# Performance work log

Measured on AMD Instinct MI355X. Metric: run time of the kernel, lower is better.

## Reference

```python
import jax, jax.numpy as jnp
import numpy as np

# irreps '128x0e + 64x1o + 32x2e' as (mul, l) pairs; ir.dim = 2*l+1
IRREPS = [(128, 0), (64, 1), (32, 2)]
B, NE = 256, 400
E_DIM, FF_DIM, HID, OUT = 32, 64, 256, 1
D = sum(m * (2 * l + 1) for m, l in IRREPS)      # 480 = irreps total dim
NCOP = sum(m for m, _ in IRREPS)                 # 224 = n_copies / inv_dim
EPS = 1e-8


def _mlp3(x, W1, b1, W2, b2, W3, b3):
    # MLP(n_layers=3): Linear+SiLU, Linear+SiLU, Linear
    h = jax.nn.silu(x @ W1 + b1)
    h = jax.nn.silu(h @ W2 + b2)
    return h @ W3 + b3


def setup_inputs() -> dict:
    key = jax.random.key(0)
    ks = jax.random.split(key, 16)

    def lin(k, i, o):
        return jax.random.normal(k, (i, o), jnp.float32) / np.float32(np.sqrt(i))

    cond_dim = E_DIM + FF_DIM            # 96
    inv_in = NCOP + FF_DIM               # 288
    return {
        "h_abs_full": jax.random.normal(ks[0], (B, D), jnp.float32),
        "e_feat": jax.random.normal(ks[1], (NE, E_DIM), jnp.float32),
        "field_abs_feat": jax.random.normal(ks[2], (B, FF_DIM), jnp.float32),
        # EnergyIrrepModulation MLP: cond_dim -> HID -> HID -> NCOP
        "mW1": lin(ks[3], cond_dim, HID), "mb1": jnp.zeros((HID,), jnp.float32),
        "mW2": lin(ks[4], HID, HID),      "mb2": jnp.zeros((HID,), jnp.float32),
        "mW3": lin(ks[5], HID, NCOP),     "mb3": jnp.zeros((NCOP,), jnp.float32),
        # out_mlp: inv_dim + ff -> HID -> HID -> OUT
        "oW1": lin(ks[6], inv_in, HID),   "ob1": jnp.zeros((HID,), jnp.float32),
        "oW2": lin(ks[7], HID, HID),      "ob2": jnp.zeros((HID,), jnp.float32),
        "oW3": lin(ks[8], HID, OUT),      "ob3": jnp.zeros((OUT,), jnp.float32),
    }


def reference(h_abs_full, e_feat, field_abs_feat,
              mW1, mb1, mW2, mb2, mW3, mb3,
              oW1, ob1, oW2, ob2, oW3, ob3):
    Bn = h_abs_full.shape[0]
    nE = e_feat.shape[0]
    ff = field_abs_feat.shape[-1]

    # cond: [B, nE, e_dim + ff]
    cond = jnp.concatenate([
        jnp.broadcast_to(e_feat[None], (Bn, nE, e_feat.shape[-1])),
        jnp.broadcast_to(field_abs_feat[:, None], (Bn, nE, ff)),
    ], axis=-1)

    # gates: [B, nE, n_copies]
    gates = _mlp3(cond, mW1, mb1, mW2, mb2, mW3, mb3)

    # Fused per-irrep broadcast gating + invariant (L2-norm) reduction.
    # h_mod[b,e, block] = x[b, block] * gate[b,e, copy]; inv = sqrt(mean(h_mod^2, dim) + eps)
    outs = []
    xoff, goff = 0, 0
    for mul, l in IRREPS:
        dim = 2 * l + 1
        xb = h_abs_full[:, xoff:xoff + mul * dim].reshape(Bn, 1, mul, dim)
        gb = gates[:, :, goff:goff + mul][..., None]          # [B, nE, mul, 1]
        m = xb * gb                                           # [B, nE, mul, dim]
        if l == 0:
            outs.append(m[..., 0])                            # scalars pass through
        else:
            outs.append(jnp.sqrt(jnp.mean(m * m, axis=-1) + EPS))
        xoff += mul * dim
        goff += mul

    inv = jnp.concatenate(
        outs + [jnp.broadcast_to(field_abs_feat[:, None], (Bn, nE, ff))], axis=-1
    )  # [B, nE, n_copies + ff]

    return _mlp3(inv, oW1, ob1, oW2, ob2, oW3, ob3)           # [B, nE, out_dim]
```

## Files before the change

kernel.cpp:

```cpp
#include <hip/hip_runtime.h>
#include <math.h>

#define BB 256
#define NE 400
#define NP (BB * NE)
#define HID 256
#define NCOP 224
#define DIN 480
#define MBLK 64
#define NBLK (NP / MBLK)

typedef _Float16 half8 __attribute__((ext_vector_type(8)));
typedef _Float16 half4 __attribute__((ext_vector_type(4)));
typedef float f4 __attribute__((ext_vector_type(4)));

static __device__ __forceinline__ float silu_f(float x) {
    return x / (1.0f + __expf(-x));
}

static __device__ __forceinline__ int swz(int row, int colbyte) {
    return (row * 512 + colbyte) ^ ((row & 7) << 4);
}

__global__ void precompute_kernel(const float* __restrict__ h_abs,
                                  const float* __restrict__ e_feat,
                                  const float* __restrict__ field,
                                  const float* __restrict__ mW1,
                                  const float* __restrict__ mb1,
                                  const float* __restrict__ oW1,
                                  const float* __restrict__ ob1,
                                  float* __restrict__ E1,
                                  float* __restrict__ F1,
                                  float* __restrict__ Fo,
                                  float* __restrict__ S)
{
    int r = blockIdx.x;
    int t = threadIdx.x;
    if (r < NE) {
        float a = 0.f;
        #pragma unroll
        for (int k = 0; k < 32; ++k) a += e_feat[r * 32 + k] * mW1[k * HID + t];
        E1[r * HID + t] = a;
    } else if (r < NE + BB) {
        int b = r - NE;
        float a = mb1[t];
        #pragma unroll
        for (int k = 0; k < 64; ++k) a += field[b * 64 + k] * mW1[(32 + k) * HID + t];
        F1[b * HID + t] = a;
    } else if (r < NE + 2 * BB) {
        int b = r - NE - BB;
        float a = ob1[t];
        #pragma unroll
        for (int k = 0; k < 64; ++k) a += field[b * 64 + k] * oW1[(224 + k) * HID + t];
        Fo[b * HID + t] = a;
    } else {
        int b = r - NE - 2 * BB;
        if (t < 64) {
            const float* x = h_abs + b * DIN + 128 + t * 3;
            S[b * 96 + t] = (x[0]*x[0] + x[1]*x[1] + x[2]*x[2]) * (1.0f / 3.0f);
        } else if (t < 96) {
            int c = t - 64;
            const float* x = h_abs + b * DIN + 320 + c * 5;
            float s = 0.f;
            #pragma unroll
            for (int d = 0; d < 5; ++d) s += x[d] * x[d];
            S[b * 96 + t] = s * 0.2f;
        }
    }
}

__global__ void pack_weights(const float* __restrict__ mW2, const float* __restrict__ mW3,
                             const float* __restrict__ oW1, const float* __restrict__ oW2,
                             _Float16* __restrict__ PB2, _Float16* __restrict__ PB3,
                             _Float16* __restrict__ PO1, _Float16* __restrict__ PO2)
{
    int blk = blockIdx.x;
    int l = threadIdx.x;
    const float* W; _Float16* P; int LD;
    if (blk < 128)      { W = mW2; P = PB2; LD = 256; }
    else if (blk < 240) { blk -= 128; W = mW3; P = PB3; LD = 224; }
    else if (blk < 352) { blk -= 240; W = oW1; P = PO1; LD = 256; }
    else                { blk -= 352; W = oW2; P = PO2; LD = 256; }
    int KST = (P == PO1) ? 7 : 8;
    int nt = blk / KST, ks = blk - nt * KST;
    int n  = nt * 16 + (l & 15);
    int k0 = ks * 32 + (l >> 4) * 8;
    half8 v;
    #pragma unroll
    for (int j = 0; j < 8; ++j) v[j] = (_Float16)W[(size_t)(k0 + j) * LD + n];
    *(half8*)&P[(size_t)(blk * 64 + l) * 8] = v;
}

template<int KST, bool TWO>
static __device__ __forceinline__ void mma_phase(const half8* __restrict__ Wp,
                                                 const char* actp, int lane,
                                                 int tile0, f4 acc[4][2])
{
    half8 bf0[KST], bf1[TWO ? KST : 1];
    #pragma unroll
    for (int ks = 0; ks < KST; ++ks)
        bf0[ks] = Wp[(tile0 * KST + ks) * 64 + lane];
    if (TWO) {
        #pragma unroll
        for (int ks = 0; ks < KST; ++ks)
            bf1[ks] = Wp[((tile0 + 8) * KST + ks) * 64 + lane];
    }

    #pragma unroll
    for (int mt = 0; mt < 4; ++mt) {
        acc[mt][0] = (f4){0.f, 0.f, 0.f, 0.f};
        acc[mt][1] = (f4){0.f, 0.f, 0.f, 0.f};
    }

    #pragma unroll
    for (int ks = 0; ks < KST; ++ks) {
        int kb = ks * 64 + ((lane >> 4) << 4);
        half8 a[4];
        #pragma unroll
        for (int mt = 0; mt < 4; ++mt) {
            int row = mt * 16 + (lane & 15);
            a[mt] = *(const half8*)(actp + ((row * 512 + kb) ^ ((row & 7) << 4)));
        }
        #pragma unroll
        for (int mt = 0; mt < 4; ++mt)
            acc[mt][0] = __builtin_amdgcn_mfma_f32_16x16x32_f16(bf0[ks], a[mt], acc[mt][0], 0, 0, 0);
        if (TWO) {
            #pragma unroll
            for (int mt = 0; mt < 4; ++mt)
                acc[mt][1] = __builtin_amdgcn_mfma_f32_16x16x32_f16(bf1[ks], a[mt], acc[mt][1], 0, 0, 0);
        }
    }
}

__global__ __launch_bounds__(512, 1)
void fused_mfma(const float* __restrict__ h_abs,
                const float* __restrict__ mb2, const float* __restrict__ mb3,
                const float* __restrict__ ob2,
                const float* __restrict__ oW3, const float* __restrict__ ob3,
                const float* __restrict__ E1, const float* __restrict__ F1,
                const float* __restrict__ Fo, const float* __restrict__ S,
                const half8* __restrict__ PB2, const half8* __restrict__ PB3,
                const half8* __restrict__ PO1, const half8* __restrict__ PO2,
                float* __restrict__ out)
{
    __shared__ char act[MBLK * 512];
    __shared__ float sred[8][64];

    const int t    = threadIdx.x;
    const int lane = t & 63;
    const int w    = t >> 6;
    const int p0   = blockIdx.x * MBLK;
    const int lr   = lane & 15;
    const int lq   = lane >> 4;

    const int b0 = p0 / NE;
    const int r0 = p0 - b0 * NE;

    {
        #pragma unroll
        for (int i = 0; i < 4; ++i) {
            int c   = i * 512 + t;
            int row = c >> 5;
            int c0  = (c & 31) * 8;
            int e = r0 + row;
            int b = b0;
            if (e >= NE) { e -= NE; b += 1; }
            const f4* ep = (const f4*)&E1[e * HID + c0];
            const f4* fp = (const f4*)&F1[b * HID + c0];
            f4 e0 = ep[0], e1 = ep[1];
            f4 f0 = fp[0], f1 = fp[1];
            half8 hv;
            #pragma unroll
            for (int j = 0; j < 4; ++j) hv[j]     = (_Float16)silu_f(e0[j] + f0[j]);
            #pragma unroll
            for (int j = 0; j < 4; ++j) hv[4 + j] = (_Float16)silu_f(e1[j] + f1[j]);
            *(half8*)(act + swz(row, c0 * 2)) = hv;
        }
    }
    __syncthreads();

    f4 acc[4][2];

    mma_phase<8, true>(PB2, act, lane, w, acc);
    __syncthreads();
    #pragma unroll
    for (int ntj = 0; ntj < 2; ++ntj) {
        int n0 = (w + ntj * 8) * 16 + lq * 4;
        f4 bias = *(const f4*)&mb2[n0];
        #pragma unroll
        for (int mt = 0; mt < 4; ++mt) {
            int row = mt * 16 + lr;
            half4 hv;
            #pragma unroll
            for (int r = 0; r < 4; ++r)
                hv[r] = (_Float16)silu_f(acc[mt][ntj][r] + bias[r]);
            *(half4*)(act + swz(row, n0 * 2)) = hv;
        }
    }
    __syncthreads();

    if (w < 6) mma_phase<8, true >(PB3, act, lane, w, acc);
    else       mma_phase<8, false>(PB3, act, lane, w, acc);
    __syncthreads();
    #pragma unroll
    for (int ntj = 0; ntj < 2; ++ntj) {
        int tile = w + ntj * 8;
        if (tile < 14) {
            int n0 = tile * 16 + lq * 4;
            f4 bias = *(const f4*)&mb3[n0];
            #pragma unroll
            for (int mt = 0; mt < 4; ++mt) {
                int row = mt * 16 + lr;
                int b = b0 + ((r0 + row) >= NE);
                half4 hv;
                if (n0 < 128) {
                    f4 xh = *(const f4*)&h_abs[b * DIN + n0];
                    #pragma unroll
                    for (int r = 0; r < 4; ++r)
                        hv[r] = (_Float16)(xh[r] * (acc[mt][ntj][r] + bias[r]));
                } else {
                    f4 sv = *(const f4*)&S[b * 96 + (n0 - 128)];
                    #pragma unroll
                    for (int r = 0; r < 4; ++r) {
                        float g = acc[mt][ntj][r] + bias[r];
                        hv[r] = (_Float16)sqrtf(g * g * sv[r] + 1e-8f);
                    }
                }
                *(half4*)(act + swz(row, n0 * 2)) = hv;
            }
        }
    }
    __syncthreads();

    mma_phase<7, true>(PO1, act, lane, w, acc);
    __syncthreads();
    #pragma unroll
    for (int ntj = 0; ntj < 2; ++ntj) {
        int n0 = (w + ntj * 8) * 16 + lq * 4;
        #pragma unroll
        for (int mt = 0; mt < 4; ++mt) {
            int row = mt * 16 + lr;
            int b = b0 + ((r0 + row) >= NE);
            f4 fo = *(const f4*)&Fo[b * HID + n0];
            half4 hv;
            #pragma unroll
            for (int r = 0; r < 4; ++r)
                hv[r] = (_Float16)silu_f(acc[mt][ntj][r] + fo[r]);
            *(half4*)(act + swz(row, n0 * 2)) = hv;
        }
    }
    __syncthreads();

    mma_phase<8, true>(PO2, act, lane, w, acc);
    {
        float partial[4] = {0.f, 0.f, 0.f, 0.f};
        #pragma unroll
        for (int ntj = 0; ntj < 2; ++ntj) {
            int n0 = (w + ntj * 8) * 16 + lq * 4;
            f4 bias = *(const f4*)&ob2[n0];
            f4 wv   = *(const f4*)&oW3[n0];
            #pragma unroll
            for (int mt = 0; mt < 4; ++mt)
                #pragma unroll
                for (int r = 0; r < 4; ++r)
                    partial[mt] += silu_f(acc[mt][ntj][r] + bias[r]) * wv[r];
        }
        #pragma unroll
        for (int mt = 0; mt < 4; ++mt) {
            float s = partial[mt];
            s += __shfl_xor(s, 16, 64);
            s += __shfl_xor(s, 32, 64);
            if (lq == 0) sred[w][mt * 16 + lr] = s;
        }
    }
    __syncthreads();
    if (t < 64) {
        float s = ob3[0];
        #pragma unroll
        for (int ww = 0; ww < 8; ++ww) s += sred[ww][t];
        out[p0 + t] = s;
    }
}

extern "C" void kernel_launch(void* const* d_in, const int* in_sizes, int n_in,
                              void* d_out, int out_size, void* d_ws, size_t ws_size,
                              hipStream_t stream) {
    const float* h_abs  = (const float*)d_in[0];
    const float* e_feat = (const float*)d_in[1];
    const float* field  = (const float*)d_in[2];
    const float* mW1 = (const float*)d_in[3];
    const float* mb1 = (const float*)d_in[4];
    const float* mW2 = (const float*)d_in[5];
    const float* mb2 = (const float*)d_in[6];
    const float* mW3 = (const float*)d_in[7];
    const float* mb3 = (const float*)d_in[8];
    const float* oW1 = (const float*)d_in[9];
    const float* ob1 = (const float*)d_in[10];
    const float* oW2 = (const float*)d_in[11];
    const float* ob2 = (const float*)d_in[12];
    const float* oW3 = (const float*)d_in[13];
    const float* ob3 = (const float*)d_in[14];
    float* out = (float*)d_out;

    float* ws = (float*)d_ws;
    float* E1 = ws;
    float* F1 = E1 + NE * HID;
    float* Fo = F1 + BB * HID;
    float* S  = Fo + BB * HID;
    _Float16* PB2 = (_Float16*)(S + BB * 96);
    _Float16* PB3 = PB2 + 16 * 8 * 64 * 8;
    _Float16* PO1 = PB3 + 14 * 8 * 64 * 8;
    _Float16* PO2 = PO1 + 16 * 7 * 64 * 8;

    precompute_kernel<<<NE + 3 * BB, 256, 0, stream>>>(
        h_abs, e_feat, field, mW1, mb1, oW1, ob1, E1, F1, Fo, S);

    pack_weights<<<480, 64, 0, stream>>>(
        mW2, mW3, oW1, oW2, PB2, PB3, PO1, PO2);

    fused_mfma<<<NBLK, 512, 0, stream>>>(
        h_abs, mb2, mb3, ob2, oW3, ob3,
        E1, F1, Fo, S,
        (const half8*)PB2, (const half8*)PB3, (const half8*)PO1, (const half8*)PO2,
        out);
}
```

Before: 111.5 us.

## Halve row tile to 32 with 4-wave blocks and fold biases into accumulators

Each block now handles 32 rows instead of 64, using 256 threads (4 waves) instead of 512. Each wave computes 4 output column tiles over 2 row tiles, in two MFMA passes per layer. Bias and Fo values are loaded straight into the accumulators before the MFMAs, which removes the separate zeroing and the bias adds in the epilogues. The aim is more blocks for better load balance and lower LDS use, at the cost of twice as many weight-fragment reads per output row, since each block reuses weights over fewer rows.

```diff
diff --git a/kernel.cpp b/kernel.cpp
--- a/kernel.cpp
+++ b/kernel.cpp
@@ -7,7 +7,7 @@
 #define HID 256
 #define NCOP 224
 #define DIN 480
-#define MBLK 64
+#define MBLK 32
 #define NBLK (NP / MBLK)
 
 typedef _Float16 half8 __attribute__((ext_vector_type(8)));
@@ -92,47 +92,41 @@
 }
 
 template<int KST, bool TWO>
-static __device__ __forceinline__ void mma_phase(const half8* __restrict__ Wp,
-                                                 const char* actp, int lane,
-                                                 int tile0, f4 acc[4][2])
+static __device__ __forceinline__ void mma_pass(const half8* __restrict__ Wp,
+                                                const char* actp, int lane,
+                                                int tileA, f4 acc[2][2])
 {
-    half8 bf0[KST], bf1[TWO ? KST : 1];
+    half8 bfA[KST], bfB[TWO ? KST : 1];
     #pragma unroll
     for (int ks = 0; ks < KST; ++ks)
-        bf0[ks] = Wp[(tile0 * KST + ks) * 64 + lane];
+        bfA[ks] = Wp[(tileA * KST + ks) * 64 + lane];
     if (TWO) {
         #pragma unroll
         for (int ks = 0; ks < KST; ++ks)
-            bf1[ks] = Wp[((tile0 + 8) * KST + ks) * 64 + lane];
-    }
-
-    #pragma unroll
-    for (int mt = 0; mt < 4; ++mt) {
-        acc[mt][0] = (f4){0.f, 0.f, 0.f, 0.f};
-        acc[mt][1] = (f4){0.f, 0.f, 0.f, 0.f};
+            bfB[ks] = Wp[((tileA + 4) * KST + ks) * 64 + lane];
     }
 
     #pragma unroll
     for (int ks = 0; ks < KST; ++ks) {
         int kb = ks * 64 + ((lane >> 4) << 4);
-        half8 a[4];
-        #pragma unroll
-        for (int mt = 0; mt < 4; ++mt) {
+        half8 a[2];
+        #pragma unroll
+        for (int mt = 0; mt < 2; ++mt) {
             int row = mt * 16 + (lane & 15);
             a[mt] = *(const half8*)(actp + ((row * 512 + kb) ^ ((row & 7) << 4)));
         }
         #pragma unroll
-        for (int mt = 0; mt < 4; ++mt)
-            acc[mt][0] = __builtin_amdgcn_mfma_f32_16x16x32_f16(bf0[ks], a[mt], acc[mt][0], 0, 0, 0);
+        for (int mt = 0; mt < 2; ++mt)
+            acc[mt][0] = __builtin_amdgcn_mfma_f32_16x16x32_f16(bfA[ks], a[mt], acc[mt][0], 0, 0, 0);
         if (TWO) {
             #pragma unroll
-            for (int mt = 0; mt < 4; ++mt)
-                acc[mt][1] = __builtin_amdgcn_mfma_f32_16x16x32_f16(bf1[ks], a[mt], acc[mt][1], 0, 0, 0);
-        }
-    }
-}
-
-__global__ __launch_bounds__(512, 1)
+            for (int mt = 0; mt < 2; ++mt)
+                acc[mt][1] = __builtin_amdgcn_mfma_f32_16x16x32_f16(bfB[ks], a[mt], acc[mt][1], 0, 0, 0);
+        }
+    }
+}
+
+__global__ __launch_bounds__(256, 1)
 void fused_mfma(const float* __restrict__ h_abs,
                 const float* __restrict__ mb2, const float* __restrict__ mb3,
                 const float* __restrict__ ob2,
@@ -144,7 +138,7 @@
                 float* __restrict__ out)
 {
     __shared__ char act[MBLK * 512];
-    __shared__ float sred[8][64];
+    __shared__ float sred[4][32];
 
     const int t    = threadIdx.x;
     const int lane = t & 63;
@@ -159,7 +153,7 @@
     {
         #pragma unroll
         for (int i = 0; i < 4; ++i) {
-            int c   = i * 512 + t;
+            int c   = i * 256 + t;
             int row = c >> 5;
             int c0  = (c & 31) * 8;
             int e = r0 + row;
@@ -179,51 +173,71 @@
     }
     __syncthreads();
 
-    f4 acc[4][2];
-
-    mma_phase<8, true>(PB2, act, lane, w, acc);
-    __syncthreads();
-    #pragma unroll
-    for (int ntj = 0; ntj < 2; ++ntj) {
-        int n0 = (w + ntj * 8) * 16 + lq * 4;
-        f4 bias = *(const f4*)&mb2[n0];
-        #pragma unroll
-        for (int mt = 0; mt < 4; ++mt) {
+    f4 accA[2][2], accB[2][2];
+
+    #pragma unroll
+    for (int j = 0; j < 2; ++j) {
+        f4 bA = *(const f4*)&mb2[(w + 4 * j) * 16 + lq * 4];
+        f4 bB = *(const f4*)&mb2[(w + 8 + 4 * j) * 16 + lq * 4];
+        #pragma unroll
+        for (int mt = 0; mt < 2; ++mt) { accA[mt][j] = bA; accB[mt][j] = bB; }
+    }
+    mma_pass<8, true>(PB2, act, lane, w,     accA);
+    mma_pass<8, true>(PB2, act, lane, w + 8, accB);
+    __syncthreads();
+    #pragma unroll
+    for (int g = 0; g < 4; ++g) {
+        int tile = w + 4 * g;
+        const f4 (*acc)[2] = (g < 2) ? accA : accB;
+        int j = g & 1;
+        int n0 = tile * 16 + lq * 4;
+        #pragma unroll
+        for (int mt = 0; mt < 2; ++mt) {
             int row = mt * 16 + lr;
             half4 hv;
             #pragma unroll
             for (int r = 0; r < 4; ++r)
-                hv[r] = (_Float16)silu_f(acc[mt][ntj][r] + bias[r]);
+                hv[r] = (_Float16)silu_f(acc[mt][j][r]);
             *(half4*)(act + swz(row, n0 * 2)) = hv;
         }
     }
     __syncthreads();
 
-    if (w < 6) mma_phase<8, true >(PB3, act, lane, w, acc);
-    else       mma_phase<8, false>(PB3, act, lane, w, acc);
-    __syncthreads();
-    #pragma unroll
-    for (int ntj = 0; ntj < 2; ++ntj) {
-        int tile = w + ntj * 8;
+    #pragma unroll
+    for (int j = 0; j < 2; ++j) {
+        int tA = w + 4 * j, tB = w + 8 + 4 * j;
+        f4 bA = *(const f4*)&mb3[tA * 16 + lq * 4];
+        f4 bB = (tB < 14) ? *(const f4*)&mb3[tB * 16 + lq * 4] : (f4){0,0,0,0};
+        #pragma unroll
+        for (int mt = 0; mt < 2; ++mt) { accA[mt][j] = bA; accB[mt][j] = bB; }
+    }
+    mma_pass<8, true>(PB3, act, lane, w, accA);
+    if (w < 2) mma_pass<8, true >(PB3, act, lane, w + 8, accB);
+    else       mma_pass<8, false>(PB3, act, lane, w + 8, accB);
+    __syncthreads();
+    #pragma unroll
+    for (int g = 0; g < 4; ++g) {
+        int tile = w + 4 * g;
         if (tile < 14) {
+            const f4 (*acc)[2] = (g < 2) ? accA : accB;
+            int j = g & 1;
             int n0 = tile * 16 + lq * 4;
-            f4 bias = *(const f4*)&mb3[n0];
-            #pragma unroll
-            for (int mt = 0; mt < 4; ++mt) {
+            #pragma unroll
+            for (int mt = 0; mt < 2; ++mt) {
                 int row = mt * 16 + lr;
                 int b = b0 + ((r0 + row) >= NE);
                 half4 hv;
-                if (n0 < 128) {
+                if (tile < 8) {
                     f4 xh = *(const f4*)&h_abs[b * DIN + n0];
                     #pragma unroll
                     for (int r = 0; r < 4; ++r)
-                        hv[r] = (_Float16)(xh[r] * (acc[mt][ntj][r] + bias[r]));
+                        hv[r] = (_Float16)(xh[r] * acc[mt][j][r]);
                 } else {
                     f4 sv = *(const f4*)&S[b * 96 + (n0 - 128)];
                     #pragma unroll
                     for (int r = 0; r < 4; ++r) {
-                        float g = acc[mt][ntj][r] + bias[r];
-                        hv[r] = (_Float16)sqrtf(g * g * sv[r] + 1e-8f);
+                        float g2 = acc[mt][j][r];
+                        hv[r] = (_Float16)sqrtf(g2 * g2 * sv[r] + 1e-8f);
                     }
                 }
                 *(half4*)(act + swz(row, n0 * 2)) = hv;
@@ -232,41 +246,65 @@
     }
     __syncthreads();
 
-    mma_phase<7, true>(PO1, act, lane, w, acc);
-    __syncthreads();
-    #pragma unroll
-    for (int ntj = 0; ntj < 2; ++ntj) {
-        int n0 = (w + ntj * 8) * 16 + lq * 4;
-        #pragma unroll
-        for (int mt = 0; mt < 4; ++mt) {
+    {
+        int bnd[2];
+        #pragma unroll
+        for (int mt = 0; mt < 2; ++mt)
+            bnd[mt] = b0 + ((r0 + mt * 16 + lr) >= NE);
+        #pragma unroll
+        for (int j = 0; j < 2; ++j)
+            #pragma unroll
+            for (int mt = 0; mt < 2; ++mt) {
+                accA[mt][j] = *(const f4*)&Fo[bnd[mt] * HID + (w + 4 * j) * 16 + lq * 4];
+                accB[mt][j] = *(const f4*)&Fo[bnd[mt] * HID + (w + 8 + 4 * j) * 16 + lq * 4];
+            }
+    }
+    mma_pass<7, true>(PO1, act, lane, w,     accA);
+    mma_pass<7, true>(PO1, act, lane, w + 8, accB);
+    __syncthreads();
+    #pragma unroll
+    for (int g = 0; g < 4; ++g) {
+        int tile = w + 4 * g;
+        const f4 (*acc)[2] = (g < 2) ? accA : accB;
+        int j = g & 1;
+        int n0 = tile * 16 + lq * 4;
+        #pragma unroll
+        for (int mt = 0; mt < 2; ++mt) {
             int row = mt * 16 + lr;
-            int b = b0 + ((r0 + row) >= NE);
-            f4 fo = *(const f4*)&Fo[b * HID + n0];
             half4 hv;
             #pragma unroll
             for (int r = 0; r < 4; ++r)
-                hv[r] = (_Float16)silu_f(acc[mt][ntj][r] + fo[r]);
+                hv[r] = (_Float16)silu_f(acc[mt][j][r]);
             *(half4*)(act + swz(row, n0 * 2)) = hv;
         }
     }
     __syncthreads();
 
-    mma_phase<8, true>(PO2, act, lane, w, acc);
+    #pragma unroll
+    for (int j = 0; j < 2; ++j) {
+        f4 bA = *(const f4*)&ob2[(w + 4 * j) * 16 + lq * 4];
+        f4 bB = *(const f4*)&ob2[(w + 8 + 4 * j) * 16 + lq * 4];
+        #pragma unroll
+        for (int mt = 0; mt < 2; ++mt) { accA[mt][j] = bA; accB[mt][j] = bB; }
+    }
+    mma_pass<8, true>(PO2, act, lane, w,     accA);
+    mma_pass<8, true>(PO2, act, lane, w + 8, accB);
     {
-        float partial[4] = {0.f, 0.f, 0.f, 0.f};
-        #pragma unroll
-        for (int ntj = 0; ntj < 2; ++ntj) {
-            int n0 = (w + ntj * 8) * 16 + lq * 4;
-            f4 bias = *(const f4*)&ob2[n0];
-            f4 wv   = *(const f4*)&oW3[n0];
-            #pragma unroll
-            for (int mt = 0; mt < 4; ++mt)
+        float partial[2] = {0.f, 0.f};
+        #pragma unroll
+        for (int g = 0; g < 4; ++g) {
+            int n0 = (w + 4 * g) * 16 + lq * 4;
+            const f4 (*acc)[2] = (g < 2) ? accA : accB;
+            int j = g & 1;
+            f4 wv = *(const f4*)&oW3[n0];
+            #pragma unroll
+            for (int mt = 0; mt < 2; ++mt)
                 #pragma unroll
                 for (int r = 0; r < 4; ++r)
-                    partial[mt] += silu_f(acc[mt][ntj][r] + bias[r]) * wv[r];
-        }
-        #pragma unroll
-        for (int mt = 0; mt < 4; ++mt) {
+                    partial[mt] += silu_f(acc[mt][j][r]) * wv[r];
+        }
+        #pragma unroll
+        for (int mt = 0; mt < 2; ++mt) {
             float s = partial[mt];
             s += __shfl_xor(s, 16, 64);
             s += __shfl_xor(s, 32, 64);
@@ -274,10 +312,10 @@
         }
     }
     __syncthreads();
-    if (t < 64) {
+    if (t < 32) {
         float s = ob3[0];
         #pragma unroll
-        for (int ww = 0; ww < 8; ++ww) s += sred[ww][t];
+        for (int ww = 0; ww < 4; ++ww) s += sred[ww][t];
         out[p0 + t] = s;
     }
 }
@@ -318,7 +356,7 @@
     pack_weights<<<480, 64, 0, stream>>>(
         mW2, mW3, oW1, oW2, PB2, PB3, PO1, PO2);
 
-    fused_mfma<<<NBLK, 512, 0, stream>>>(
+    fused_mfma<<<NBLK, 256, 0, stream>>>(
         h_abs, mb2, mb3, ob2, oW3, ob3,
         E1, F1, Fo, S,
         (const half8*)PB2, (const half8*)PB3, (const half8*)PO1, (const half8*)PO2,
```

Result: slower. 126.2 us (+13.2%).

## Double row tile to 128 with 1024-thread blocks and bias-initialized accumulators

Applied to the files above, without the earlier changes.

Each block now handles 128 rows using 16 waves. Waves are paired so that two of them share each column tile, each working on its own 64-row half of the activation buffer. Biases and the Fo term are loaded straight into the MFMA accumulators instead of being added in the epilogues, and the reduction scratch now reuses the activation LDS. The aim is to halve the number of blocks and the weight reloads per row and to trim epilogue arithmetic, at the cost of a larger LDS footprint and 1024-thread blocks, which may reduce scheduling flexibility.

```diff
diff --git a/kernel.cpp b/kernel.cpp
--- a/kernel.cpp
+++ b/kernel.cpp
@@ -7,7 +7,7 @@
 #define HID 256
 #define NCOP 224
 #define DIN 480
-#define MBLK 64
+#define MBLK 128
 #define NBLK (NP / MBLK)
 
 typedef _Float16 half8 __attribute__((ext_vector_type(8)));
@@ -107,12 +107,6 @@
     }
 
     #pragma unroll
-    for (int mt = 0; mt < 4; ++mt) {
-        acc[mt][0] = (f4){0.f, 0.f, 0.f, 0.f};
-        acc[mt][1] = (f4){0.f, 0.f, 0.f, 0.f};
-    }
-
-    #pragma unroll
     for (int ks = 0; ks < KST; ++ks) {
         int kb = ks * 64 + ((lane >> 4) << 4);
         half8 a[4];
@@ -132,7 +126,7 @@
     }
 }
 
-__global__ __launch_bounds__(512, 1)
+__global__ __launch_bounds__(1024, 1)
 void fused_mfma(const float* __restrict__ h_abs,
                 const float* __restrict__ mb2, const float* __restrict__ mb3,
                 const float* __restrict__ ob2,
@@ -144,14 +138,17 @@
                 float* __restrict__ out)
 {
     __shared__ char act[MBLK * 512];
-    __shared__ float sred[8][64];
+    float* sred = (float*)act;
 
     const int t    = threadIdx.x;
     const int lane = t & 63;
     const int w    = t >> 6;
+    const int wh   = w & 1;
+    const int wc   = w >> 1;
     const int p0   = blockIdx.x * MBLK;
     const int lr   = lane & 15;
     const int lq   = lane >> 4;
+    const char* actw = act + wh * 64 * 512;
 
     const int b0 = p0 / NE;
     const int r0 = p0 - b0 * NE;
@@ -159,7 +156,7 @@
     {
         #pragma unroll
         for (int i = 0; i < 4; ++i) {
-            int c   = i * 512 + t;
+            int c   = i * 1024 + t;
             int row = c >> 5;
             int c0  = (c & 31) * 8;
             int e = r0 + row;
@@ -181,48 +178,59 @@
 
     f4 acc[4][2];
 
-    mma_phase<8, true>(PB2, act, lane, w, acc);
-    __syncthreads();
-    #pragma unroll
-    for (int ntj = 0; ntj < 2; ++ntj) {
-        int n0 = (w + ntj * 8) * 16 + lq * 4;
-        f4 bias = *(const f4*)&mb2[n0];
+    #pragma unroll
+    for (int ntj = 0; ntj < 2; ++ntj) {
+        f4 bias = *(const f4*)&mb2[(wc + ntj * 8) * 16 + lq * 4];
+        #pragma unroll
+        for (int mt = 0; mt < 4; ++mt) acc[mt][ntj] = bias;
+    }
+    mma_phase<8, true>(PB2, actw, lane, wc, acc);
+    __syncthreads();
+    #pragma unroll
+    for (int ntj = 0; ntj < 2; ++ntj) {
+        int n0 = (wc + ntj * 8) * 16 + lq * 4;
         #pragma unroll
         for (int mt = 0; mt < 4; ++mt) {
-            int row = mt * 16 + lr;
+            int row = wh * 64 + mt * 16 + lr;
             half4 hv;
             #pragma unroll
             for (int r = 0; r < 4; ++r)
-                hv[r] = (_Float16)silu_f(acc[mt][ntj][r] + bias[r]);
+                hv[r] = (_Float16)silu_f(acc[mt][ntj][r]);
             *(half4*)(act + swz(row, n0 * 2)) = hv;
         }
     }
     __syncthreads();
 
-    if (w < 6) mma_phase<8, true >(PB3, act, lane, w, acc);
-    else       mma_phase<8, false>(PB3, act, lane, w, acc);
-    __syncthreads();
-    #pragma unroll
-    for (int ntj = 0; ntj < 2; ++ntj) {
-        int tile = w + ntj * 8;
+    #pragma unroll
+    for (int ntj = 0; ntj < 2; ++ntj) {
+        int tile = wc + ntj * 8;
+        f4 bias = (tile < 14) ? *(const f4*)&mb3[tile * 16 + lq * 4] : (f4){0,0,0,0};
+        #pragma unroll
+        for (int mt = 0; mt < 4; ++mt) acc[mt][ntj] = bias;
+    }
+    if (wc < 6) mma_phase<8, true >(PB3, actw, lane, wc, acc);
+    else        mma_phase<8, false>(PB3, actw, lane, wc, acc);
+    __syncthreads();
+    #pragma unroll
+    for (int ntj = 0; ntj < 2; ++ntj) {
+        int tile = wc + ntj * 8;
         if (tile < 14) {
             int n0 = tile * 16 + lq * 4;
-            f4 bias = *(const f4*)&mb3[n0];
             #pragma unroll
             for (int mt = 0; mt < 4; ++mt) {
-                int row = mt * 16 + lr;
+                int row = wh * 64 + mt * 16 + lr;
                 int b = b0 + ((r0 + row) >= NE);
                 half4 hv;
-                if (n0 < 128) {
+                if (tile < 8) {
                     f4 xh = *(const f4*)&h_abs[b * DIN + n0];
                     #pragma unroll
                     for (int r = 0; r < 4; ++r)
-                        hv[r] = (_Float16)(xh[r] * (acc[mt][ntj][r] + bias[r]));
+                        hv[r] = (_Float16)(xh[r] * acc[mt][ntj][r]);
                 } else {
                     f4 sv = *(const f4*)&S[b * 96 + (n0 - 128)];
                     #pragma unroll
                     for (int r = 0; r < 4; ++r) {
-                        float g = acc[mt][ntj][r] + bias[r];
+                        float g = acc[mt][ntj][r];
                         hv[r] = (_Float16)sqrtf(g * g * sv[r] + 1e-8f);
                     }
                 }
@@ -232,52 +240,69 @@
     }
     __syncthreads();
 
-    mma_phase<7, true>(PO1, act, lane, w, acc);
-    __syncthreads();
-    #pragma unroll
-    for (int ntj = 0; ntj < 2; ++ntj) {
-        int n0 = (w + ntj * 8) * 16 + lq * 4;
+    {
+        int bnd[4];
+        #pragma unroll
+        for (int mt = 0; mt < 4; ++mt)
+            bnd[mt] = b0 + ((r0 + wh * 64 + mt * 16 + lr) >= NE);
+        #pragma unroll
+        for (int ntj = 0; ntj < 2; ++ntj) {
+            int n0 = (wc + ntj * 8) * 16 + lq * 4;
+            #pragma unroll
+            for (int mt = 0; mt < 4; ++mt)
+                acc[mt][ntj] = *(const f4*)&Fo[bnd[mt] * HID + n0];
+        }
+    }
+    mma_phase<7, true>(PO1, actw, lane, wc, acc);
+    __syncthreads();
+    #pragma unroll
+    for (int ntj = 0; ntj < 2; ++ntj) {
+        int n0 = (wc + ntj * 8) * 16 + lq * 4;
         #pragma unroll
         for (int mt = 0; mt < 4; ++mt) {
-            int row = mt * 16 + lr;
-            int b = b0 + ((r0 + row) >= NE);
-            f4 fo = *(const f4*)&Fo[b * HID + n0];
+            int row = wh * 64 + mt * 16 + lr;
             half4 hv;
             #pragma unroll
             for (int r = 0; r < 4; ++r)
-                hv[r] = (_Float16)silu_f(acc[mt][ntj][r] + fo[r]);
+                hv[r] = (_Float16)silu_f(acc[mt][ntj][r]);
             *(half4*)(act + swz(row, n0 * 2)) = hv;
         }
     }
     __syncthreads();
 
-    mma_phase<8, true>(PO2, act, lane, w, acc);
+    #pragma unroll
+    for (int ntj = 0; ntj < 2; ++ntj) {
+        f4 bias = *(const f4*)&ob2[(wc + ntj * 8) * 16 + lq * 4];
+        #pragma unroll
+        for (int mt = 0; mt < 4; ++mt) acc[mt][ntj] = bias;
+    }
+    mma_phase<8, true>(PO2, actw, lane, wc, acc);
     {
         float partial[4] = {0.f, 0.f, 0.f, 0.f};
         #pragma unroll
         for (int ntj = 0; ntj < 2; ++ntj) {
-            int n0 = (w + ntj * 8) * 16 + lq * 4;
-            f4 bias = *(const f4*)&ob2[n0];
-            f4 wv   = *(const f4*)&oW3[n0];
+            int n0 = (wc + ntj * 8) * 16 + lq * 4;
+            f4 wv = *(const f4*)&oW3[n0];
             #pragma unroll
             for (int mt = 0; mt < 4; ++mt)
                 #pragma unroll
                 for (int r = 0; r < 4; ++r)
-                    partial[mt] += silu_f(acc[mt][ntj][r] + bias[r]) * wv[r];
-        }
+                    partial[mt] += silu_f(acc[mt][ntj][r]) * wv[r];
+        }
+        __syncthreads();
         #pragma unroll
         for (int mt = 0; mt < 4; ++mt) {
             float s = partial[mt];
             s += __shfl_xor(s, 16, 64);
             s += __shfl_xor(s, 32, 64);
-            if (lq == 0) sred[w][mt * 16 + lr] = s;
-        }
-    }
-    __syncthreads();
-    if (t < 64) {
+            if (lq == 0) sred[wc * 128 + wh * 64 + mt * 16 + lr] = s;
+        }
+    }
+    __syncthreads();
+    if (t < 128) {
         float s = ob3[0];
         #pragma unroll
-        for (int ww = 0; ww < 8; ++ww) s += sred[ww][t];
+        for (int ww = 0; ww < 8; ++ww) s += sred[ww * 128 + t];
         out[p0 + t] = s;
     }
 }
@@ -318,7 +343,7 @@
     pack_weights<<<480, 64, 0, stream>>>(
         mW2, mW3, oW1, oW2, PB2, PB3, PO1, PO2);
 
-    fused_mfma<<<NBLK, 512, 0, stream>>>(
+    fused_mfma<<<NBLK, 1024, 0, stream>>>(
         h_abs, mb2, mb3, ob2, oW3, ob3,
         E1, F1, Fo, S,
         (const half8*)PB2, (const half8*)PB3, (const half8*)PO1, (const half8*)PO2,
```

Result: slower. 128.8 us (+15.5%).
